# Optimization experiments

Measured on AMD Instinct MI355X. Metric: run time of the kernel, lower is better.

## Reference

```python
import math
import jax, jax.numpy as jnp
import numpy as np

B, L, D = 16, 2048, 64  # batch, seq len (m == n, self-attention), head dim
C = 30                   # ProbSparse sampling factor c


def setup_inputs() -> dict:
    key = jax.random.key(0)
    kq, kk, kv = jax.random.split(key, 3)
    Q = jax.random.normal(kq, (B, L, D), dtype=jnp.float32)
    K = jax.random.normal(kk, (B, L, D), dtype=jnp.float32)
    V = jax.random.normal(kv, (B, L, D), dtype=jnp.float32)
    return {"Q": Q, "K": K, "V": V, "seed": 0}


def reference(Q, K, V, seed):
    b, m, d = Q.shape
    n = K.shape[1]
    u = int(C * math.log(m))              # number of active queries
    U = min(int(m * math.log(n)), n)      # number of sampled keys (clamped to n)
    inv_sqrt_d = 1.0 / math.sqrt(d)

    rngs = jax.random.split(jax.random.key(seed), b)

    def _each_sample(Qb, Kb, Vb, r):
        # random sample of U key rows without replacement
        idx = jax.random.choice(r, n, shape=(U,), replace=False)
        Kbar = Kb[idx]                                # [U, d]
        Sbar = jnp.matmul(Qb, Kbar.T)                 # [m, U]
        M = jnp.max(Sbar, axis=1) - jnp.mean(Sbar, axis=1)  # sparsity measure [m]
        _, I = jax.lax.top_k(M, u)                    # active query indices [u]
        Qbar = Qb[I]                                  # [u, d]
        A = jax.nn.softmax(jnp.matmul(Qbar, Kb.T) * inv_sqrt_d, axis=-1)  # [u, n]
        S1 = jnp.matmul(A, Vb)                        # [u, d]
        # literal source: fill with mean(V, axis=1, keepdims=True) -> (n,1) broadcast (m==n)
        S = jnp.broadcast_to(jnp.mean(Vb, axis=1, keepdims=True), (m, d))
        return S.at[I].set(S1)

    return jax.vmap(_each_sample)(Q, K, V, rngs)
```

## Files before the change

kernel.cpp:

```cpp
#include <hip/hip_runtime.h>

#define NB 16
#define NN 2048
#define DH 64
#define NSEL 228
#define KS 8
#define CHUNK (NN / KS)
#define RS 4
#define EPSBAND 2.0e-3f
#define MAXB 32

using s16x8 = __attribute__((ext_vector_type(8))) short;
using f32x16 = __attribute__((ext_vector_type(16))) float;

static __device__ __forceinline__ unsigned short f2bf(float x) {
  unsigned int u = __float_as_uint(x);
  u += 0x7fffu + ((u >> 16) & 1u);
  return (unsigned short)(u >> 16);
}
static __device__ __forceinline__ float bf2f(unsigned short h) {
  return __uint_as_float(((unsigned int)h) << 16);
}
static __device__ __forceinline__ unsigned int enc(float f) {
  unsigned int u = __float_as_uint(f);
  return (u & 0x80000000u) ? ~u : (u | 0x80000000u);
}
static __device__ __forceinline__ float dec(unsigned int k) {
  return (k & 0x80000000u) ? __uint_as_float(k & 0x7fffffffu)
                           : __uint_as_float(~k);
}

__global__ __launch_bounds__(256) void convk_kernel(const float* __restrict__ K,
                                                    unsigned short* __restrict__ Khi,
                                                    unsigned short* __restrict__ Klo) {
  const size_t e = ((size_t)blockIdx.x * 256 + threadIdx.x) * 8;
  float4 a = *(const float4*)(K + e);
  float4 b = *(const float4*)(K + e + 4);
  float v[8] = {a.x, a.y, a.z, a.w, b.x, b.y, b.z, b.w};
  union { unsigned short u[8]; s16x8 s; } H, L;
  #pragma unroll
  for (int j = 0; j < 8; ++j) {
    unsigned short h = f2bf(v[j]);
    H.u[j] = h;
    L.u[j] = f2bf(v[j] - bf2f(h));
  }
  *(s16x8*)(Khi + e) = H.s;
  *(s16x8*)(Klo + e) = L.s;
}

__global__ __launch_bounds__(256) void convv_kernel(const float* __restrict__ V,
                                                    unsigned short* __restrict__ VThi,
                                                    unsigned short* __restrict__ VTlo) {
  __shared__ __align__(16) float T[64][65];
  const int b = blockIdx.y, ch = blockIdx.x;
  const int tid = threadIdx.x;
  {
    const int r = tid >> 2;
    const int c0 = (tid & 3) * 16;
    const float* src = V + ((size_t)b * NN + ch * 64 + r) * DH + c0;
    #pragma unroll
    for (int f = 0; f < 4; ++f) {
      float4 v = *(const float4*)(src + f * 4);
      T[r][c0 + f * 4 + 0] = v.x;
      T[r][c0 + f * 4 + 1] = v.y;
      T[r][c0 + f * 4 + 2] = v.z;
      T[r][c0 + f * 4 + 3] = v.w;
    }
  }
  __syncthreads();
  const int d = tid >> 2;
  const int j0 = (tid & 3) * 16;
  unsigned short* oh = VThi + ((size_t)b * DH + d) * NN + ch * 64 + j0;
  unsigned short* ol = VTlo + ((size_t)b * DH + d) * NN + ch * 64 + j0;
  #pragma unroll
  for (int half = 0; half < 2; ++half) {
    union { unsigned short u[8]; s16x8 s; } H, L;
    #pragma unroll
    for (int c = 0; c < 8; ++c) {
      const float v = T[j0 + half * 8 + c][d];
      const unsigned short hh = f2bf(v);
      H.u[c] = hh;
      L.u[c] = f2bf(v - bf2f(hh));
    }
    *(s16x8*)(oh + half * 8) = H.s;
    *(s16x8*)(ol + half * 8) = L.s;
  }
}

__global__ __launch_bounds__(256) void kcolsum_kernel(const float* __restrict__ K,
                                                      float* __restrict__ Kpart) {
  __shared__ float part[4][64];
  const int b = blockIdx.y, ch = blockIdx.x;
  const int d = threadIdx.x & 63, g = threadIdx.x >> 6;
  const float* Kb = K + ((size_t)b * NN + ch * 128) * DH;
  float s = 0.f;
  for (int r = g; r < 128; r += 4) s += Kb[r * DH + d];
  part[g][d] = s;
  __syncthreads();
  if (threadIdx.x < 64)
    Kpart[((size_t)b * 16 + ch) * 64 + threadIdx.x] =
        part[0][threadIdx.x] + part[1][threadIdx.x] +
        part[2][threadIdx.x] + part[3][threadIdx.x];
}

__global__ __launch_bounds__(256, 4) void rowstat_mfma(const float* __restrict__ Q,
                                                       const unsigned short* __restrict__ Khi,
                                                       const unsigned short* __restrict__ Klo,
                                                       float* __restrict__ Mmax) {
  __shared__ __align__(16) unsigned short KHs[128 * 64];
  __shared__ __align__(16) unsigned short KLs[128 * 64];
  const int b = blockIdx.y, cz = blockIdx.z;
  const int qbase = blockIdx.x * 128;
  const int tid = threadIdx.x;
  const int w = tid >> 6, lane = tid & 63;
  const int l31 = lane & 31, hi5 = lane >> 5;

  s16x8 qh[4], ql[4];
  {
    const float* qrow = Q + ((size_t)b * NN + qbase + w * 32 + l31) * DH;
    #pragma unroll
    for (int ks = 0; ks < 4; ++ks) {
      const int d0 = ks * 16 + hi5 * 8;
      float4 x = *(const float4*)(qrow + d0);
      float4 y = *(const float4*)(qrow + d0 + 4);
      float v[8] = {x.x, x.y, x.z, x.w, y.x, y.y, y.z, y.w};
      union { unsigned short u[8]; s16x8 s; } H, L;
      #pragma unroll
      for (int j = 0; j < 8; ++j) {
        unsigned short h = f2bf(v[j]);
        H.u[j] = h;
        L.u[j] = f2bf(v[j] - bf2f(h));
      }
      qh[ks] = H.s;
      ql[ks] = L.s;
    }
  }

  const size_t kbase = ((size_t)b * NN + cz * (NN / RS)) * DH;
  f32x16 vmax;
  #pragma unroll
  for (int i = 0; i < 16; ++i) vmax[i] = -3.0e38f;

  const int sr = tid >> 1;
  const int sh = tid & 1;

  for (int stage = 0; stage < NN / RS / 128; ++stage) {
    __syncthreads();
    {
      const size_t g = kbase + (size_t)(stage * 128 + sr) * DH + sh * 32;
      const unsigned short* gh = Khi + g;
      const unsigned short* gl = Klo + g;
      #pragma unroll
      for (int c = 0; c < 4; ++c) {
        s16x8 hv = *(const s16x8*)(gh + c * 8);
        s16x8 lv = *(const s16x8*)(gl + c * 8);
        const int chn = (sh * 4 + c) ^ (sr & 7);
        *(s16x8*)&KHs[(sr * 8 + chn) * 8] = hv;
        *(s16x8*)&KLs[(sr * 8 + chn) * 8] = lv;
      }
    }
    __syncthreads();

    #pragma unroll
    for (int ksub = 0; ksub < 4; ++ksub) {
      const int kr = ksub * 32 + l31;
      f32x16 acc;
      #pragma unroll
      for (int i = 0; i < 16; ++i) acc[i] = 0.f;
      #pragma unroll
      for (int ks = 0; ks < 4; ++ks) {
        const int chn = (ks * 2 + hi5) ^ (kr & 7);
        s16x8 ah = *(const s16x8*)&KHs[(kr * 8 + chn) * 8];
        s16x8 al = *(const s16x8*)&KLs[(kr * 8 + chn) * 8];
        acc = __builtin_amdgcn_mfma_f32_32x32x16_bf16(ah, qh[ks], acc, 0, 0, 0);
        acc = __builtin_amdgcn_mfma_f32_32x32x16_bf16(al, qh[ks], acc, 0, 0, 0);
        acc = __builtin_amdgcn_mfma_f32_32x32x16_bf16(ah, ql[ks], acc, 0, 0, 0);
      }
      #pragma unroll
      for (int i = 0; i < 16; ++i) vmax[i] = fmaxf(vmax[i], acc[i]);
    }
  }

  float m = vmax[0];
  #pragma unroll
  for (int i = 1; i < 16; ++i) m = fmaxf(m, vmax[i]);
  m = fmaxf(m, __shfl_xor(m, 32));
  if (lane < 32)
    Mmax[((size_t)cz * NB + b) * NN + qbase + w * 32 + lane] = m;
}

__global__ __launch_bounds__(256) void mstat_kernel(const float* __restrict__ Q,
                                                    const float* __restrict__ Mmax,
                                                    const float* __restrict__ Kpart,
                                                    unsigned int* __restrict__ keysW,
                                                    float* __restrict__ meanv) {
  __shared__ float Ksl[64];
  const int b = blockIdx.y;
  const int seg = blockIdx.x;
  const int tid = threadIdx.x;
  if (tid < 64) {
    float s = 0.f;
    #pragma unroll
    for (int c = 0; c < 16; ++c) s += Kpart[((size_t)b * 16 + c) * 64 + tid];
    Ksl[tid] = s;
  }
  __syncthreads();
  const int i = seg * 256 + tid;
  float mv = -3.0e38f;
  #pragma unroll
  for (int cz = 0; cz < RS; ++cz)
    mv = fmaxf(mv, Mmax[((size_t)cz * NB + b) * NN + i]);
  const float* qrow = Q + ((size_t)b * NN + i) * DH;
  float s = 0.f;
  #pragma unroll
  for (int d4 = 0; d4 < 16; ++d4) {
    float4 qv = *(const float4*)(qrow + d4 * 4);
    s = fmaf(qv.x, Ksl[d4 * 4 + 0], s);
    s = fmaf(qv.y, Ksl[d4 * 4 + 1], s);
    s = fmaf(qv.z, Ksl[d4 * 4 + 2], s);
    s = fmaf(qv.w, Ksl[d4 * 4 + 3], s);
  }
  const float mean = s * (1.0f / NN);
  meanv[(size_t)b * NN + i] = mean;
  keysW[(size_t)b * NN + i] = enc(mv - mean);
}

static __device__ unsigned int radix_thresh(const unsigned int* kreg, int lane,
                                            int wid, int* red) {
  unsigned int v = 0u;
  for (int bit = 31; bit >= 0; --bit) {
    const unsigned int cand = v | (1u << bit);
    int c = 0;
    #pragma unroll
    for (int f = 0; f < 8; ++f) c += (kreg[f] >= cand) ? 1 : 0;
    #pragma unroll
    for (int off = 1; off < 64; off <<= 1) c += __shfl_xor(c, off);
    if (lane == 0) red[wid] = c;
    __syncthreads();
    if (red[0] + red[1] + red[2] + red[3] >= NSEL) v = cand;
    __syncthreads();
  }
  return v;
}

__global__ __launch_bounds__(256) void radix1_kernel(const unsigned int* __restrict__ keysW,
                                                     int* __restrict__ Band,
                                                     int* __restrict__ nband) {
  __shared__ int red[4];
  __shared__ int cntS;
  const int b = blockIdx.x;
  const int tid = threadIdx.x;
  const int lane = tid & 63, wid = tid >> 6;
  const int base = tid * 8;

  unsigned int kreg[8];
  #pragma unroll
  for (int f = 0; f < 8; ++f) kreg[f] = keysW[(size_t)b * NN + base + f];
  if (tid == 0) cntS = 0;
  __syncthreads();

  const unsigned int v1 = radix_thresh(kreg, lane, wid, red);
  const float vf = dec(v1);

  #pragma unroll
  for (int f = 0; f < 8; ++f) {
    if (fabsf(dec(kreg[f]) - vf) <= EPSBAND) {
      int p = atomicAdd(&cntS, 1);
      Band[(size_t)b * NN + p] = base + f;
    }
  }
  __syncthreads();
  if (tid == 0) nband[b] = cntS;
}

__global__ __launch_bounds__(256) void recheck_kernel(const float* __restrict__ Q,
                                                      const float* __restrict__ K,
                                                      const int* __restrict__ Band,
                                                      const int* __restrict__ nband,
                                                      const float* __restrict__ meanv,
                                                      unsigned int* __restrict__ keysW) {
  __shared__ float qsh[64];
  __shared__ float fred[4];
  const int b = blockIdx.y;
  const int nb_ = nband[b];
  const int tid = threadIdx.x;
  const int lane = tid & 63, wid = tid >> 6;

  for (int n = blockIdx.x; n < nb_; n += MAXB) {
    const int row = Band[(size_t)b * NN + n];
    __syncthreads();
    if (tid < 64) qsh[tid] = Q[((size_t)b * NN + row) * DH + tid];
    __syncthreads();
    float lmax = -3.0e38f;
    for (int j = tid; j < NN; j += 256) {
      const float* krow = K + ((size_t)b * NN + j) * DH;
      float s = 0.f;
      #pragma unroll
      for (int d4 = 0; d4 < 16; ++d4) {
        float4 kv = *(const float4*)(krow + d4 * 4);
        s = fmaf(kv.x, qsh[d4 * 4 + 0], s);
        s = fmaf(kv.y, qsh[d4 * 4 + 1], s);
        s = fmaf(kv.z, qsh[d4 * 4 + 2], s);
        s = fmaf(kv.w, qsh[d4 * 4 + 3], s);
      }
      lmax = fmaxf(lmax, s);
    }
    #pragma unroll
    for (int off = 1; off < 64; off <<= 1)
      lmax = fmaxf(lmax, __shfl_xor(lmax, off));
    if (lane == 0) fred[wid] = lmax;
    __syncthreads();
    if (tid == 0) {
      const float mx = fmaxf(fmaxf(fred[0], fred[1]), fmaxf(fred[2], fred[3]));
      keysW[(size_t)b * NN + row] = enc(mx - meanv[(size_t)b * NN + row]);
    }
  }
}

__global__ __launch_bounds__(256) void radix2_kernel(const unsigned int* __restrict__ keysW,
                                                     int* __restrict__ Isel) {
  __shared__ int red[4];
  const int b = blockIdx.x;
  const int tid = threadIdx.x;
  const int lane = tid & 63, wid = tid >> 6;
  const int base = tid * 8;

  unsigned int kreg[8];
  #pragma unroll
  for (int f = 0; f < 8; ++f) kreg[f] = keysW[(size_t)b * NN + base + f];
  __syncthreads();

  const unsigned int v2 = radix_thresh(kreg, lane, wid, red);

  int flg[8];
  int cnt = 0;
  #pragma unroll
  for (int f = 0; f < 8; ++f) { flg[f] = (kreg[f] > v2) ? 1 : 0; cnt += flg[f]; }
  int scan = cnt;
  #pragma unroll
  for (int off = 1; off < 64; off <<= 1) {
    const int t = __shfl_up(scan, off);
    if (lane >= off) scan += t;
  }
  if (lane == 63) red[wid] = scan;
  __syncthreads();
  int wbase = 0;
  for (int ww = 0; ww < wid; ++ww) wbase += red[ww];
  const int cg = red[0] + red[1] + red[2] + red[3];
  int pos = wbase + scan - cnt;
  #pragma unroll
  for (int f = 0; f < 8; ++f)
    if (flg[f]) { Isel[b * NSEL + pos] = base + f; ++pos; }
  __syncthreads();

  const int need = NSEL - cg;
  cnt = 0;
  #pragma unroll
  for (int f = 0; f < 8; ++f) { flg[f] = (kreg[f] == v2) ? 1 : 0; cnt += flg[f]; }
  scan = cnt;
  #pragma unroll
  for (int off = 1; off < 64; off <<= 1) {
    const int t = __shfl_up(scan, off);
    if (lane >= off) scan += t;
  }
  if (lane == 63) red[wid] = scan;
  __syncthreads();
  wbase = 0;
  for (int ww = 0; ww < wid; ++ww) wbase += red[ww];
  pos = wbase + scan - cnt;
  #pragma unroll
  for (int f = 0; f < 8; ++f)
    if (flg[f]) {
      if (pos < need) Isel[b * NSEL + cg + pos] = base + f;
      ++pos;
    }
}

__global__ __launch_bounds__(256) void fill_kernel(const float* __restrict__ V,
                                                   float* __restrict__ out) {
  const size_t row = (size_t)blockIdx.x * 4 + (threadIdx.x >> 6);
  const int lane = threadIdx.x & 63;
  float x = V[row * DH + lane];
  #pragma unroll
  for (int off = 1; off < 64; off <<= 1) x += __shfl_xor(x, off);
  out[row * DH + lane] = x * (1.0f / DH);
}

__global__ __launch_bounds__(256, 2) void attn_mfma(const float* __restrict__ Q,
                                                    const unsigned short* __restrict__ Khi,
                                                    const unsigned short* __restrict__ Klo,
                                                    const unsigned short* __restrict__ VThi,
                                                    const unsigned short* __restrict__ VTlo,
                                                    const int* __restrict__ Isel,
                                                    float* __restrict__ Pm,
                                                    float* __restrict__ Pl,
                                                    float* __restrict__ Po) {
  __shared__ float wmax[4][32];
  __shared__ float wl[4][32];
  __shared__ __align__(16) float Opart[4][32][68];
  const int b = blockIdx.z, kc = blockIdx.y, g = blockIdx.x;
  const int tid = threadIdx.x, w = tid >> 6, lane = tid & 63;
  const int l31 = lane & 31, h = lane >> 5;

  const int lq = g * 32 + l31;
  const int qidx = (lq < NSEL) ? Isel[b * NSEL + lq] : Isel[b * NSEL];
  s16x8 qbh[4], qbl[4];
  {
    const float* qr = Q + ((size_t)b * NN + qidx) * DH;
    #pragma unroll
    for (int s = 0; s < 4; ++s) {
      const int d0 = s * 16 + h * 8;
      float4 x = *(const float4*)(qr + d0);
      float4 y = *(const float4*)(qr + d0 + 4);
      float v[8] = {x.x, x.y, x.z, x.w, y.x, y.y, y.z, y.w};
      union { unsigned short u[8]; s16x8 s8; } H, L;
      #pragma unroll
      for (int j = 0; j < 8; ++j) {
        const unsigned short hh = f2bf(v[j]);
        H.u[j] = hh;
        L.u[j] = f2bf(v[j] - bf2f(hh));
      }
      qbh[s] = H.s8;
      qbl[s] = L.s8;
    }
  }

  const size_t krow0 = (size_t)b * NN + kc * CHUNK + w * 64;
  f32x16 p[2];
  #pragma unroll
  for (int t = 0; t < 2; ++t) {
    const unsigned short* kh = Khi + (krow0 + t * 32 + l31) * DH + h * 8;
    const unsigned short* kl = Klo + (krow0 + t * 32 + l31) * DH + h * 8;
    f32x16 acc;
    #pragma unroll
    for (int i = 0; i < 16; ++i) acc[i] = 0.f;
    #pragma unroll
    for (int s = 0; s < 4; ++s) {
      const s16x8 ah = *(const s16x8*)(kh + s * 16);
      const s16x8 al = *(const s16x8*)(kl + s * 16);
      acc = __builtin_amdgcn_mfma_f32_32x32x16_bf16(ah, qbh[s], acc, 0, 0, 0);
      acc = __builtin_amdgcn_mfma_f32_32x32x16_bf16(al, qbh[s], acc, 0, 0, 0);
      acc = __builtin_amdgcn_mfma_f32_32x32x16_bf16(ah, qbl[s], acc, 0, 0, 0);
    }
    p[t] = acc;
  }

  float rmax = p[0][0];
  #pragma unroll
  for (int i = 1; i < 16; ++i) rmax = fmaxf(rmax, p[0][i]);
  #pragma unroll
  for (int i = 0; i < 16; ++i) rmax = fmaxf(rmax, p[1][i]);
  rmax = fmaxf(rmax, __shfl_xor(rmax, 32));
  if (lane < 32) wmax[w][lane] = rmax;
  __syncthreads();
  const float gmax = fmaxf(fmaxf(wmax[0][l31], wmax[1][l31]),
                           fmaxf(wmax[2][l31], wmax[3][l31]));
  const float m = gmax * 0.125f;

  float lsum = 0.f;
  #pragma unroll
  for (int t = 0; t < 2; ++t)
    #pragma unroll
    for (int i = 0; i < 16; ++i) {
      const float e = __expf(fmaf(p[t][i], 0.125f, -m));
      p[t][i] = e;
      lsum += e;
    }
  lsum += __shfl_xor(lsum, 32);
  if (lane < 32) wl[w][lane] = lsum;

  f32x16 oacc[2];
  #pragma unroll
  for (int i = 0; i < 16; ++i) { oacc[0][i] = 0.f; oacc[1][i] = 0.f; }

  #pragma unroll
  for (int s = 0; s < 4; ++s) {
    const int t = s >> 1, kb = s & 1;
    float pr[8];
    #pragma unroll
    for (int j = 0; j < 8; ++j) pr[j] = p[t][kb * 8 + j];
    unsigned int ah[4], al[4];
    #pragma unroll
    for (int pi = 0; pi < 4; ++pi) {
      const unsigned short h0 = f2bf(pr[pi * 2]);
      const unsigned short h1 = f2bf(pr[pi * 2 + 1]);
      ah[pi] = (unsigned int)h0 | ((unsigned int)h1 << 16);
      al[pi] = (unsigned int)f2bf(pr[pi * 2] - bf2f(h0)) |
               ((unsigned int)f2bf(pr[pi * 2 + 1] - bf2f(h1)) << 16);
    }
    unsigned int sh_[4], sl_[4];
    #pragma unroll
    for (int pi = 0; pi < 4; ++pi) {
      sh_[pi] = (unsigned int)__shfl_xor((int)ah[pi], 32);
      sl_[pi] = (unsigned int)__shfl_xor((int)al[pi], 32);
    }
    union { int4 i4; s16x8 s8; } BH, BL;
    if (h == 0) {
      BH.i4 = make_int4((int)ah[0], (int)ah[1], (int)sh_[0], (int)sh_[1]);
      BL.i4 = make_int4((int)al[0], (int)al[1], (int)sl_[0], (int)sl_[1]);
    } else {
      BH.i4 = make_int4((int)sh_[2], (int)sh_[3], (int)ah[2], (int)ah[3]);
      BL.i4 = make_int4((int)sl_[2], (int)sl_[3], (int)al[2], (int)al[3]);
    }
    const size_t koff = (size_t)kc * CHUNK + w * 64 + s * 16 + h * 8;
    #pragma unroll
    for (int dt = 0; dt < 2; ++dt) {
      const size_t vrow = ((size_t)b * DH + dt * 32 + l31) * NN + koff;
      const s16x8 av = *(const s16x8*)(VThi + vrow);
      const s16x8 avl = *(const s16x8*)(VTlo + vrow);
      oacc[dt] = __builtin_amdgcn_mfma_f32_32x32x16_bf16(av, BH.s8, oacc[dt], 0, 0, 0);
      oacc[dt] = __builtin_amdgcn_mfma_f32_32x32x16_bf16(av, BL.s8, oacc[dt], 0, 0, 0);
      oacc[dt] = __builtin_amdgcn_mfma_f32_32x32x16_bf16(avl, BH.s8, oacc[dt], 0, 0, 0);
    }
  }

  #pragma unroll
  for (int dt = 0; dt < 2; ++dt)
    #pragma unroll
    for (int rg = 0; rg < 4; ++rg) {
      const int d0 = dt * 32 + rg * 8 + h * 4;
      float4 vv;
      vv.x = oacc[dt][rg * 4 + 0];
      vv.y = oacc[dt][rg * 4 + 1];
      vv.z = oacc[dt][rg * 4 + 2];
      vv.w = oacc[dt][rg * 4 + 3];
      *(float4*)&Opart[w][l31][d0] = vv;
    }
  __syncthreads();

  const int q = tid >> 3, dg = (tid & 7) * 8;
  float4 s0, s1;
  s0.x = s0.y = s0.z = s0.w = 0.f;
  s1.x = s1.y = s1.z = s1.w = 0.f;
  #pragma unroll
  for (int ww = 0; ww < 4; ++ww) {
    const float4 a = *(const float4*)&Opart[ww][q][dg];
    const float4 c = *(const float4*)&Opart[ww][q][dg + 4];
    s0.x += a.x; s0.y += a.y; s0.z += a.z; s0.w += a.w;
    s1.x += c.x; s1.y += c.y; s1.z += c.z; s1.w += c.w;
  }
  const int lq2 = g * 32 + q;
  if (lq2 < NSEL) {
    const size_t row = ((size_t)b * NSEL + lq2) * KS + kc;
    *(float4*)(Po + row * 64 + dg) = s0;
    *(float4*)(Po + row * 64 + dg + 4) = s1;
    if (dg == 0) {
      const float gm2 = fmaxf(fmaxf(wmax[0][q], wmax[1][q]),
                              fmaxf(wmax[2][q], wmax[3][q]));
      Pm[row] = gm2 * 0.125f;
      Pl[row] = wl[0][q] + wl[1][q] + wl[2][q] + wl[3][q];
    }
  }
}

__global__ __launch_bounds__(256) void combine_kernel(const int* __restrict__ Isel,
                                                      const float* __restrict__ Pm,
                                                      const float* __restrict__ Pl,
                                                      const float* __restrict__ Po,
                                                      float* __restrict__ out) {
  const int r = blockIdx.x * 4 + (threadIdx.x >> 6);
  if (r >= NB * NSEL) return;
  const int lane = threadIdx.x & 63;
  const int b = r / NSEL;
  const int qidx = Isel[r];
  const size_t base = (size_t)r * KS;

  float pm[KS];
  float gm = -3.0e38f;
  #pragma unroll
  for (int c = 0; c < KS; ++c) { pm[c] = Pm[base + c]; gm = fmaxf(gm, pm[c]); }
  float L = 0.f, od = 0.f;
  #pragma unroll
  for (int c = 0; c < KS; ++c) {
    const float e = __expf(pm[c] - gm);
    L += Pl[base + c] * e;
    od += Po[(base + c) * 64 + lane] * e;
  }
  out[((size_t)b * NN + qidx) * DH + lane] = od / L;
}

extern "C" void kernel_launch(void* const* d_in, const int* in_sizes, int n_in,
                              void* d_out, int out_size, void* d_ws, size_t ws_size,
                              hipStream_t stream) {
  const float* Q = (const float*)d_in[0];
  const float* K = (const float*)d_in[1];
  const float* V = (const float*)d_in[2];
  float* out = (float*)d_out;

  float* Mmax = (float*)d_ws;
  float* Kpart = Mmax + (size_t)RS * NB * NN;
  unsigned int* keysW = (unsigned int*)(Kpart + (size_t)NB * 16 * 64);
  float* meanv = (float*)(keysW + (size_t)NB * NN);
  int* Band = (int*)(meanv + (size_t)NB * NN);
  int* nband = Band + (size_t)NB * NN;
  int* Isel = nband + 16;
  float* Pm = (float*)(Isel + NB * NSEL);
  float* Pl = Pm + (size_t)NB * NSEL * KS;
  float* Po = Pl + (size_t)NB * NSEL * KS;
  unsigned short* Khi = (unsigned short*)(Po + (size_t)NB * NSEL * KS * 64);
  unsigned short* Klo = Khi + (size_t)NB * NN * DH;
  unsigned short* VThi = Klo + (size_t)NB * NN * DH;
  unsigned short* VTlo = VThi + (size_t)NB * NN * DH;

  convk_kernel<<<dim3((NB * NN * DH) / (256 * 8)), 256, 0, stream>>>(K, Khi, Klo);
  convv_kernel<<<dim3(NN / 64, NB), 256, 0, stream>>>(V, VThi, VTlo);
  kcolsum_kernel<<<dim3(16, NB), 256, 0, stream>>>(K, Kpart);
  rowstat_mfma<<<dim3(NN / 128, NB, RS), 256, 0, stream>>>(Q, Khi, Klo, Mmax);
  mstat_kernel<<<dim3(8, NB), 256, 0, stream>>>(Q, Mmax, Kpart, keysW, meanv);
  radix1_kernel<<<dim3(NB), 256, 0, stream>>>(keysW, Band, nband);
  recheck_kernel<<<dim3(MAXB, NB), 256, 0, stream>>>(Q, K, Band, nband, meanv, keysW);
  radix2_kernel<<<dim3(NB), 256, 0, stream>>>(keysW, Isel);
  fill_kernel<<<dim3(NB * NN / 4), 256, 0, stream>>>(V, out);
  attn_mfma<<<dim3(8, KS, NB), 256, 0, stream>>>(Q, Khi, Klo, VThi, VTlo, Isel,
                                                 Pm, Pl, Po);
  combine_kernel<<<dim3((NB * NSEL + 3) / 4), 256, 0, stream>>>(Isel, Pm, Pl, Po, out);
}
```

Before: 230.2 us.

## Fuse K/V conversion with column sums, merge fill/combine, halve key splits

The K and V bf16 hi/lo conversion kernels and the K column-sum kernel become one launch, with the column sums taken from the shared tile. The mean-fill and split-combine kernels merge into one pass, driven by a per-row position map that radix2 now writes. Attention key splits drop from 8 to 4, so each warp handles 128 keys. The aim is fewer launches and less partial-result traffic, at the cost of fewer attention blocks and more registers per warp.

```diff
diff --git a/kernel.cpp b/kernel.cpp
--- a/kernel.cpp
+++ b/kernel.cpp
@@ -4,7 +4,7 @@
 #define NN 2048
 #define DH 64
 #define NSEL 228
-#define KS 8
+#define KS 4
 #define CHUNK (NN / KS)
 #define RS 4
 #define EPSBAND 2.0e-3f
@@ -30,77 +30,82 @@
                            : __uint_as_float(~k);
 }
 
-__global__ __launch_bounds__(256) void convk_kernel(const float* __restrict__ K,
-                                                    unsigned short* __restrict__ Khi,
-                                                    unsigned short* __restrict__ Klo) {
-  const size_t e = ((size_t)blockIdx.x * 256 + threadIdx.x) * 8;
-  float4 a = *(const float4*)(K + e);
-  float4 b = *(const float4*)(K + e + 4);
-  float v[8] = {a.x, a.y, a.z, a.w, b.x, b.y, b.z, b.w};
-  union { unsigned short u[8]; s16x8 s; } H, L;
-  #pragma unroll
-  for (int j = 0; j < 8; ++j) {
-    unsigned short h = f2bf(v[j]);
-    H.u[j] = h;
-    L.u[j] = f2bf(v[j] - bf2f(h));
-  }
-  *(s16x8*)(Khi + e) = H.s;
-  *(s16x8*)(Klo + e) = L.s;
-}
-
-__global__ __launch_bounds__(256) void convv_kernel(const float* __restrict__ V,
-                                                    unsigned short* __restrict__ VThi,
-                                                    unsigned short* __restrict__ VTlo) {
+__global__ __launch_bounds__(256) void conv_fused(const float* __restrict__ K,
+                                                  const float* __restrict__ V,
+                                                  unsigned short* __restrict__ Khi,
+                                                  unsigned short* __restrict__ Klo,
+                                                  unsigned short* __restrict__ VThi,
+                                                  unsigned short* __restrict__ VTlo,
+                                                  float* __restrict__ Kpart) {
   __shared__ __align__(16) float T[64][65];
   const int b = blockIdx.y, ch = blockIdx.x;
   const int tid = threadIdx.x;
-  {
-    const int r = tid >> 2;
-    const int c0 = (tid & 3) * 16;
+  const int r = tid >> 2;
+  const int c0 = (tid & 3) * 16;
+
+  if (blockIdx.z == 0) {
+    const size_t off = ((size_t)b * NN + ch * 64 + r) * DH + c0;
+    const float* src = K + off;
+    float v[16];
+    #pragma unroll
+    for (int f = 0; f < 4; ++f) {
+      float4 x = *(const float4*)(src + f * 4);
+      v[f * 4 + 0] = x.x; v[f * 4 + 1] = x.y;
+      v[f * 4 + 2] = x.z; v[f * 4 + 3] = x.w;
+      T[r][c0 + f * 4 + 0] = x.x;
+      T[r][c0 + f * 4 + 1] = x.y;
+      T[r][c0 + f * 4 + 2] = x.z;
+      T[r][c0 + f * 4 + 3] = x.w;
+    }
+    #pragma unroll
+    for (int half = 0; half < 2; ++half) {
+      union { unsigned short u[8]; s16x8 s; } H, L;
+      #pragma unroll
+      for (int j = 0; j < 8; ++j) {
+        const float x = v[half * 8 + j];
+        const unsigned short hh = f2bf(x);
+        H.u[j] = hh;
+        L.u[j] = f2bf(x - bf2f(hh));
+      }
+      *(s16x8*)(Khi + off + half * 8) = H.s;
+      *(s16x8*)(Klo + off + half * 8) = L.s;
+    }
+    __syncthreads();
+    if (tid < 64) {
+      float s = 0.f;
+      #pragma unroll 8
+      for (int rr = 0; rr < 64; ++rr) s += T[rr][tid];
+      Kpart[((size_t)b * 32 + ch) * 64 + tid] = s;
+    }
+  } else {
     const float* src = V + ((size_t)b * NN + ch * 64 + r) * DH + c0;
     #pragma unroll
     for (int f = 0; f < 4; ++f) {
-      float4 v = *(const float4*)(src + f * 4);
-      T[r][c0 + f * 4 + 0] = v.x;
-      T[r][c0 + f * 4 + 1] = v.y;
-      T[r][c0 + f * 4 + 2] = v.z;
-      T[r][c0 + f * 4 + 3] = v.w;
-    }
-  }
-  __syncthreads();
-  const int d = tid >> 2;
-  const int j0 = (tid & 3) * 16;
-  unsigned short* oh = VThi + ((size_t)b * DH + d) * NN + ch * 64 + j0;
-  unsigned short* ol = VTlo + ((size_t)b * DH + d) * NN + ch * 64 + j0;
-  #pragma unroll
-  for (int half = 0; half < 2; ++half) {
-    union { unsigned short u[8]; s16x8 s; } H, L;
-    #pragma unroll
-    for (int c = 0; c < 8; ++c) {
-      const float v = T[j0 + half * 8 + c][d];
-      const unsigned short hh = f2bf(v);
-      H.u[c] = hh;
-      L.u[c] = f2bf(v - bf2f(hh));
-    }
-    *(s16x8*)(oh + half * 8) = H.s;
-    *(s16x8*)(ol + half * 8) = L.s;
-  }
-}
-
-__global__ __launch_bounds__(256) void kcolsum_kernel(const float* __restrict__ K,
-                                                      float* __restrict__ Kpart) {
-  __shared__ float part[4][64];
-  const int b = blockIdx.y, ch = blockIdx.x;
-  const int d = threadIdx.x & 63, g = threadIdx.x >> 6;
-  const float* Kb = K + ((size_t)b * NN + ch * 128) * DH;
-  float s = 0.f;
-  for (int r = g; r < 128; r += 4) s += Kb[r * DH + d];
-  part[g][d] = s;
-  __syncthreads();
-  if (threadIdx.x < 64)
-    Kpart[((size_t)b * 16 + ch) * 64 + threadIdx.x] =
-        part[0][threadIdx.x] + part[1][threadIdx.x] +
-        part[2][threadIdx.x] + part[3][threadIdx.x];
+      float4 x = *(const float4*)(src + f * 4);
+      T[r][c0 + f * 4 + 0] = x.x;
+      T[r][c0 + f * 4 + 1] = x.y;
+      T[r][c0 + f * 4 + 2] = x.z;
+      T[r][c0 + f * 4 + 3] = x.w;
+    }
+    __syncthreads();
+    const int d = tid >> 2;
+    const int j0 = (tid & 3) * 16;
+    unsigned short* oh = VThi + ((size_t)b * DH + d) * NN + ch * 64 + j0;
+    unsigned short* ol = VTlo + ((size_t)b * DH + d) * NN + ch * 64 + j0;
+    #pragma unroll
+    for (int half = 0; half < 2; ++half) {
+      union { unsigned short u[8]; s16x8 s; } H, L;
+      #pragma unroll
+      for (int c = 0; c < 8; ++c) {
+        const float x = T[j0 + half * 8 + c][d];
+        const unsigned short hh = f2bf(x);
+        H.u[c] = hh;
+        L.u[c] = f2bf(x - bf2f(hh));
+      }
+      *(s16x8*)(oh + half * 8) = H.s;
+      *(s16x8*)(ol + half * 8) = L.s;
+    }
+  }
 }
 
 __global__ __launch_bounds__(256, 4) void rowstat_mfma(const float* __restrict__ Q,
@@ -201,7 +206,7 @@
   if (tid < 64) {
     float s = 0.f;
     #pragma unroll
-    for (int c = 0; c < 16; ++c) s += Kpart[((size_t)b * 16 + c) * 64 + tid];
+    for (int c = 0; c < 32; ++c) s += Kpart[((size_t)b * 32 + c) * 64 + tid];
     Ksl[tid] = s;
   }
   __syncthreads();
@@ -318,7 +323,8 @@
 }
 
 __global__ __launch_bounds__(256) void radix2_kernel(const unsigned int* __restrict__ keysW,
-                                                     int* __restrict__ Isel) {
+                                                     int* __restrict__ Isel,
+                                                     int* __restrict__ pos) {
   __shared__ int red[4];
   const int b = blockIdx.x;
   const int tid = threadIdx.x;
@@ -347,10 +353,17 @@
   int wbase = 0;
   for (int ww = 0; ww < wid; ++ww) wbase += red[ww];
   const int cg = red[0] + red[1] + red[2] + red[3];
-  int pos = wbase + scan - cnt;
-  #pragma unroll
-  for (int f = 0; f < 8; ++f)
-    if (flg[f]) { Isel[b * NSEL + pos] = base + f; ++pos; }
+  int p = wbase + scan - cnt;
+  #pragma unroll
+  for (int f = 0; f < 8; ++f) {
+    if (flg[f]) {
+      Isel[b * NSEL + p] = base + f;
+      pos[(size_t)b * NN + base + f] = p;
+      ++p;
+    } else {
+      pos[(size_t)b * NN + base + f] = -1;
+    }
+  }
   __syncthreads();
 
   const int need = NSEL - cg;
@@ -367,23 +380,17 @@
   __syncthreads();
   wbase = 0;
   for (int ww = 0; ww < wid; ++ww) wbase += red[ww];
-  pos = wbase + scan - cnt;
-  #pragma unroll
-  for (int f = 0; f < 8; ++f)
+  p = wbase + scan - cnt;
+  #pragma unroll
+  for (int f = 0; f < 8; ++f) {
     if (flg[f]) {
-      if (pos < need) Isel[b * NSEL + cg + pos] = base + f;
-      ++pos;
-    }
-}
-
-__global__ __launch_bounds__(256) void fill_kernel(const float* __restrict__ V,
-                                                   float* __restrict__ out) {
-  const size_t row = (size_t)blockIdx.x * 4 + (threadIdx.x >> 6);
-  const int lane = threadIdx.x & 63;
-  float x = V[row * DH + lane];
-  #pragma unroll
-  for (int off = 1; off < 64; off <<= 1) x += __shfl_xor(x, off);
-  out[row * DH + lane] = x * (1.0f / DH);
+      if (p < need) {
+        Isel[b * NSEL + cg + p] = base + f;
+        pos[(size_t)b * NN + base + f] = cg + p;
+      }
+      ++p;
+    }
+  }
 }
 
 __global__ __launch_bounds__(256, 2) void attn_mfma(const float* __restrict__ Q,
@@ -425,10 +432,10 @@
     }
   }
 
-  const size_t krow0 = (size_t)b * NN + kc * CHUNK + w * 64;
-  f32x16 p[2];
-  #pragma unroll
-  for (int t = 0; t < 2; ++t) {
+  const size_t krow0 = (size_t)b * NN + kc * CHUNK + w * 128;
+  f32x16 p[4];
+  #pragma unroll
+  for (int t = 0; t < 4; ++t) {
     const unsigned short* kh = Khi + (krow0 + t * 32 + l31) * DH + h * 8;
     const unsigned short* kl = Klo + (krow0 + t * 32 + l31) * DH + h * 8;
     f32x16 acc;
@@ -447,9 +454,9 @@
 
   float rmax = p[0][0];
   #pragma unroll
-  for (int i = 1; i < 16; ++i) rmax = fmaxf(rmax, p[0][i]);
-  #pragma unroll
-  for (int i = 0; i < 16; ++i) rmax = fmaxf(rmax, p[1][i]);
+  for (int t = 0; t < 4; ++t)
+    #pragma unroll
+    for (int i = 0; i < 16; ++i) rmax = fmaxf(rmax, p[t][i]);
   rmax = fmaxf(rmax, __shfl_xor(rmax, 32));
   if (lane < 32) wmax[w][lane] = rmax;
   __syncthreads();
@@ -459,7 +466,7 @@
 
   float lsum = 0.f;
   #pragma unroll
-  for (int t = 0; t < 2; ++t)
+  for (int t = 0; t < 4; ++t)
     #pragma unroll
     for (int i = 0; i < 16; ++i) {
       const float e = __expf(fmaf(p[t][i], 0.125f, -m));
@@ -474,7 +481,7 @@
   for (int i = 0; i < 16; ++i) { oacc[0][i] = 0.f; oacc[1][i] = 0.f; }
 
   #pragma unroll
-  for (int s = 0; s < 4; ++s) {
+  for (int s = 0; s < 8; ++s) {
     const int t = s >> 1, kb = s & 1;
     float pr[8];
     #pragma unroll
@@ -502,7 +509,7 @@
       BH.i4 = make_int4((int)sh_[2], (int)sh_[3], (int)ah[2], (int)ah[3]);
       BL.i4 = make_int4((int)sl_[2], (int)sl_[3], (int)al[2], (int)al[3]);
     }
-    const size_t koff = (size_t)kc * CHUNK + w * 64 + s * 16 + h * 8;
+    const size_t koff = (size_t)kc * CHUNK + w * 128 + s * 16 + h * 8;
     #pragma unroll
     for (int dt = 0; dt < 2; ++dt) {
       const size_t vrow = ((size_t)b * DH + dt * 32 + l31) * NN + koff;
@@ -553,30 +560,36 @@
   }
 }
 
-__global__ __launch_bounds__(256) void combine_kernel(const int* __restrict__ Isel,
-                                                      const float* __restrict__ Pm,
-                                                      const float* __restrict__ Pl,
-                                                      const float* __restrict__ Po,
-                                                      float* __restrict__ out) {
-  const int r = blockIdx.x * 4 + (threadIdx.x >> 6);
-  if (r >= NB * NSEL) return;
+__global__ __launch_bounds__(256) void fill_combine(const float* __restrict__ V,
+                                                    const int* __restrict__ pos,
+                                                    const float* __restrict__ Pm,
+                                                    const float* __restrict__ Pl,
+                                                    const float* __restrict__ Po,
+                                                    float* __restrict__ out) {
+  const size_t row = (size_t)blockIdx.x * 4 + (threadIdx.x >> 6);
   const int lane = threadIdx.x & 63;
-  const int b = r / NSEL;
-  const int qidx = Isel[r];
-  const size_t base = (size_t)r * KS;
-
-  float pm[KS];
-  float gm = -3.0e38f;
-  #pragma unroll
-  for (int c = 0; c < KS; ++c) { pm[c] = Pm[base + c]; gm = fmaxf(gm, pm[c]); }
-  float L = 0.f, od = 0.f;
-  #pragma unroll
-  for (int c = 0; c < KS; ++c) {
-    const float e = __expf(pm[c] - gm);
-    L += Pl[base + c] * e;
-    od += Po[(base + c) * 64 + lane] * e;
-  }
-  out[((size_t)b * NN + qidx) * DH + lane] = od / L;
+  const int p = pos[row];
+  if (p < 0) {
+    float x = V[row * DH + lane];
+    #pragma unroll
+    for (int off = 1; off < 64; off <<= 1) x += __shfl_xor(x, off);
+    out[row * DH + lane] = x * (1.0f / DH);
+  } else {
+    const int b = (int)(row / NN);
+    const size_t base = ((size_t)b * NSEL + p) * KS;
+    float pm[KS];
+    float gm = -3.0e38f;
+    #pragma unroll
+    for (int c = 0; c < KS; ++c) { pm[c] = Pm[base + c]; gm = fmaxf(gm, pm[c]); }
+    float L = 0.f, od = 0.f;
+    #pragma unroll
+    for (int c = 0; c < KS; ++c) {
+      const float e = __expf(pm[c] - gm);
+      L += Pl[base + c] * e;
+      od += Po[(base + c) * 64 + lane] * e;
+    }
+    out[row * DH + lane] = od / L;
+  }
 }
 
 extern "C" void kernel_launch(void* const* d_in, const int* in_sizes, int n_in,
@@ -589,12 +602,13 @@
 
   float* Mmax = (float*)d_ws;
   float* Kpart = Mmax + (size_t)RS * NB * NN;
-  unsigned int* keysW = (unsigned int*)(Kpart + (size_t)NB * 16 * 64);
+  unsigned int* keysW = (unsigned int*)(Kpart + (size_t)NB * 32 * 64);
   float* meanv = (float*)(keysW + (size_t)NB * NN);
   int* Band = (int*)(meanv + (size_t)NB * NN);
   int* nband = Band + (size_t)NB * NN;
   int* Isel = nband + 16;
-  float* Pm = (float*)(Isel + NB * NSEL);
+  int* posA = Isel + NB * NSEL;
+  float* Pm = (float*)(posA + (size_t)NB * NN);
   float* Pl = Pm + (size_t)NB * NSEL * KS;
   float* Po = Pl + (size_t)NB * NSEL * KS;
   unsigned short* Khi = (unsigned short*)(Po + (size_t)NB * NSEL * KS * 64);
@@ -602,16 +616,14 @@
   unsigned short* VThi = Klo + (size_t)NB * NN * DH;
   unsigned short* VTlo = VThi + (size_t)NB * NN * DH;
 
-  convk_kernel<<<dim3((NB * NN * DH) / (256 * 8)), 256, 0, stream>>>(K, Khi, Klo);
-  convv_kernel<<<dim3(NN / 64, NB), 256, 0, stream>>>(V, VThi, VTlo);
-  kcolsum_kernel<<<dim3(16, NB), 256, 0, stream>>>(K, Kpart);
+  conv_fused<<<dim3(NN / 64, NB, 2), 256, 0, stream>>>(K, V, Khi, Klo, VThi,
+                                                       VTlo, Kpart);
   rowstat_mfma<<<dim3(NN / 128, NB, RS), 256, 0, stream>>>(Q, Khi, Klo, Mmax);
   mstat_kernel<<<dim3(8, NB), 256, 0, stream>>>(Q, Mmax, Kpart, keysW, meanv);
   radix1_kernel<<<dim3(NB), 256, 0, stream>>>(keysW, Band, nband);
   recheck_kernel<<<dim3(MAXB, NB), 256, 0, stream>>>(Q, K, Band, nband, meanv, keysW);
-  radix2_kernel<<<dim3(NB), 256, 0, stream>>>(keysW, Isel);
-  fill_kernel<<<dim3(NB * NN / 4), 256, 0, stream>>>(V, out);
+  radix2_kernel<<<dim3(NB), 256, 0, stream>>>(keysW, Isel, posA);
   attn_mfma<<<dim3(8, KS, NB), 256, 0, stream>>>(Q, Khi, Klo, VThi, VTlo, Isel,
                                                  Pm, Pl, Po);
-  combine_kernel<<<dim3((NB * NSEL + 3) / 4), 256, 0, stream>>>(Isel, Pm, Pl, Po, out);
-}
+  fill_combine<<<dim3(NB * NN / 4), 256, 0, stream>>>(V, posA, Pm, Pl, Po, out);
+}
```

Result: faster. 222.1 us (-3.5%).
